# Kernel optimization log

Measured on AMD Instinct MI355X. Metric: run time of the kernel, lower is better.

The kernel has to match this reference:

```python
import jax, jax.numpy as jnp
import numpy as np
from jax import lax

HEADS, DIM_HEAD, LANDMARKS, PINV_ITERS = 8, 64, 256, 6
D = 512


def layernorm(x, w, b, eps=1e-5):
    mu = x.mean(-1, keepdims=True)
    var = ((x - mu) ** 2).mean(-1, keepdims=True)
    return (x - mu) * lax.rsqrt(var + eps) * w + b


def pinv_iter(x, iters=PINV_ITERS):
    # Moore-Penrose pseudo-inverse via Newton-Schulz (lucidrains nystrom-attention)
    abs_x = jnp.abs(x)
    z = jnp.swapaxes(x, -1, -2) / (jnp.max(abs_x.sum(-1)) * jnp.max(abs_x.sum(-2)))
    I = jnp.eye(x.shape[-1], dtype=x.dtype)
    for _ in range(iters):
        xz = x @ z
        z = 0.25 * z @ (13 * I - xz @ (15 * I - xz @ (7 * I - xz)))
    return z


def nystrom_attention(x, qkv_w, out_w, out_b, res_w):
    b, n, _ = x.shape
    m = LANDMARKS
    pad = (m - n % m) % m
    xp = jnp.pad(x, ((0, 0), (pad, 0), (0, 0)))  # left-pad seq to multiple of m
    n_p = n + pad
    q, k, v = jnp.split(xp @ qkv_w, 3, axis=-1)
    split = lambda t: t.reshape(b, n_p, HEADS, DIM_HEAD).transpose(0, 2, 1, 3)
    q, k, v = split(q), split(k), split(v)  # (b, h, n_p, d)
    q = q * DIM_HEAD ** -0.5
    l = n_p // m  # tokens per landmark
    q_l = q.reshape(b, HEADS, m, l, DIM_HEAD).mean(3)  # (b, h, m, d)
    k_l = k.reshape(b, HEADS, m, l, DIM_HEAD).mean(3)
    a1 = jax.nn.softmax(jnp.einsum('bhnd,bhmd->bhnm', q, k_l), -1)  # (b,h,n_p,m)
    a2 = jax.nn.softmax(jnp.einsum('bhmd,bhld->bhml', q_l, k_l), -1)  # (b,h,m,m)
    a3 = jax.nn.softmax(jnp.einsum('bhmd,bhnd->bhmn', q_l, k), -1)  # (b,h,m,n_p)
    out = (a1 @ pinv_iter(a2)) @ (a3 @ v)  # (b,h,n_p,d)
    # depthwise residual conv over the seq dim, kernel (33,1), one per head
    res = lax.conv_general_dilated(v, res_w, (1, 1), [(16, 16), (0, 0)],
                                   dimension_numbers=('NCHW', 'OIHW', 'NCHW'),
                                   feature_group_count=HEADS)
    out = out + res
    out = out.transpose(0, 2, 1, 3).reshape(b, n_p, HEADS * DIM_HEAD)
    return (out @ out_w + out_b)[:, -n:]


def ppeg(x, Hh, Ww, w7, b7, w5, b5, w3, b3):
    B, _, C = x.shape
    cls_tok, feat = x[:, :1], x[:, 1:]
    f = feat.transpose(0, 2, 1).reshape(B, C, Hh, Ww)
    def dwconv(w, bb, p):
        return lax.conv_general_dilated(f, w, (1, 1), [(p, p), (p, p)],
                                        dimension_numbers=('NCHW', 'OIHW', 'NCHW'),
                                        feature_group_count=C) + bb[None, :, None, None]
    y = f + dwconv(w7, b7, 3) + dwconv(w5, b5, 2) + dwconv(w3, b3, 1)
    y = y.reshape(B, C, Hh * Ww).transpose(0, 2, 1)
    return jnp.concatenate([cls_tok, y], axis=1)


def setup_inputs() -> dict:
    key = jax.random.key(0)
    ks = jax.random.split(key, 16)
    E, NC, H = 1024, 4, HEADS
    f32 = jnp.float32
    rn = lambda k, shp, s=0.02: (jax.random.normal(k, shp, f32) * s)
    return {
        'x': jax.random.normal(ks[0], (1, 40960, E), f32),
        'fc1_w': rn(ks[1], (E, D)), 'fc1_b': jnp.zeros((D,), f32),
        'cls_token': jax.random.normal(ks[2], (1, 1, D), f32),
        'l1_norm_w': jnp.ones((D,), f32), 'l1_norm_b': jnp.zeros((D,), f32),
        'l1_qkv_w': rn(ks[3], (D, 3 * D)),
        'l1_out_w': rn(ks[4], (D, D)), 'l1_out_b': jnp.zeros((D,), f32),
        'l1_res_w': rn(ks[5], (H, 1, 33, 1), 0.1),
        'ppeg_w7': rn(ks[6], (D, 1, 7, 7), 0.1), 'ppeg_b7': jnp.zeros((D,), f32),
        'ppeg_w5': rn(ks[7], (D, 1, 5, 5), 0.1), 'ppeg_b5': jnp.zeros((D,), f32),
        'ppeg_w3': rn(ks[8], (D, 1, 3, 3), 0.1), 'ppeg_b3': jnp.zeros((D,), f32),
        'l2_norm_w': jnp.ones((D,), f32), 'l2_norm_b': jnp.zeros((D,), f32),
        'l2_qkv_w': rn(ks[9], (D, 3 * D)),
        'l2_out_w': rn(ks[10], (D, D)), 'l2_out_b': jnp.zeros((D,), f32),
        'l2_res_w': rn(ks[11], (H, 1, 33, 1), 0.1),
        'norm_w': jnp.ones((D,), f32), 'norm_b': jnp.zeros((D,), f32),
        'fc3_w': rn(ks[12], (D, NC)), 'fc3_b': jnp.zeros((NC,), f32),
    }


def reference(x, fc1_w, fc1_b, cls_token, l1_norm_w, l1_norm_b, l1_qkv_w, l1_out_w, l1_out_b, l1_res_w, ppeg_w7, ppeg_b7, ppeg_w5, ppeg_b5, ppeg_w3, ppeg_b3, l2_norm_w, l2_norm_b, l2_qkv_w, l2_out_w, l2_out_b, l2_res_w, norm_w, norm_b, fc3_w, fc3_b):
    B, N, E = x.shape  # (1, 40960, 1024)
    POOL_OUT = 20480
    # AdaptiveMaxPool2d((20480, E)) on a (1, N, E) tensor: max-pool seq dim N -> 20480
    ft = x.reshape(B, POOL_OUT, N // POOL_OUT, E).max(axis=2)
    ft = jax.nn.relu(ft @ fc1_w + fc1_b)  # (1, 20480, 512)
    Hn = ft.shape[1]
    _H = int(np.ceil(np.sqrt(Hn)))  # 144
    add = _H * _H - Hn  # 256
    ft = jnp.concatenate([ft, ft[:, :add]], axis=1)  # (1, 20736, 512)
    h = jnp.concatenate([jnp.broadcast_to(cls_token, (B, 1, D)), ft], axis=1)  # 20737 tokens
    h = h + nystrom_attention(layernorm(h, l1_norm_w, l1_norm_b), l1_qkv_w, l1_out_w, l1_out_b, l1_res_w)
    h = ppeg(h, _H, _H, ppeg_w7, ppeg_b7, ppeg_w5, ppeg_b5, ppeg_w3, ppeg_b3)
    h = h + nystrom_attention(layernorm(h, l2_norm_w, l2_norm_b), l2_qkv_w, l2_out_w, l2_out_b, l2_res_w)
    h = layernorm(h, norm_w, norm_b)[:, 0]
    logits = h @ fc3_w + fc3_b
    return logits, jax.nn.softmax(logits, -1), jnp.argmax(logits, -1)
```

## Files before the change

kernel.cpp:

```cpp
#include <hip/hip_runtime.h>


constexpr int D_    = 512;
constexpr int E_    = 1024;
constexpr int NTOK  = 20737;
constexpr int NP_   = 20992;
constexpr int NH_   = 8;
constexpr int HD_   = 64;
constexpr int MLM   = 256;
constexpr int LCH   = 82;
constexpr int HHW   = 144;
constexpr int NFEAT = 20736;
constexpr int PADR  = 255;
constexpr int NCH   = 41;
constexpr int CHTOK = 512;

typedef __attribute__((ext_vector_type(8))) short bf16x8;
typedef __attribute__((ext_vector_type(4))) float f32x4;

__device__ __forceinline__ unsigned short f2bf(float f){
  unsigned int u = __float_as_uint(f);
  unsigned int r = u + 0x7fffu + ((u >> 16) & 1u);
  return (unsigned short)(r >> 16);
}
__device__ __forceinline__ float bfu(unsigned short u){
  return __uint_as_float((unsigned int)u << 16);
}

__device__ __forceinline__ float waveMaxF(float v){
#pragma unroll
  for (int o = 32; o > 0; o >>= 1) v = fmaxf(v, __shfl_xor(v, o));
  return v;
}
__device__ __forceinline__ float waveSumF(float v){
#pragma unroll
  for (int o = 32; o > 0; o >>= 1) v += __shfl_xor(v, o);
  return v;
}
__device__ __forceinline__ float blockMax256(float v, float* sbuf){
  v = waveMaxF(v);
  if ((threadIdx.x & 63) == 0) sbuf[threadIdx.x >> 6] = v;
  __syncthreads();
  float r = fmaxf(fmaxf(sbuf[0], sbuf[1]), fmaxf(sbuf[2], sbuf[3]));
  __syncthreads();
  return r;
}
__device__ __forceinline__ float blockSum256(float v, float* sbuf){
  v = waveSumF(v);
  if ((threadIdx.x & 63) == 0) sbuf[threadIdx.x >> 6] = v;
  __syncthreads();
  float r = sbuf[0] + sbuf[1] + sbuf[2] + sbuf[3];
  __syncthreads();
  return r;
}

__global__ __launch_bounds__(256) void wtrans_kernel(
    const float* __restrict__ W, unsigned short* __restrict__ Wt, int K, int N){
  __shared__ float tile[32][33];
  const int kb = blockIdx.x * 32, nb = blockIdx.y * 32;
  const int tx = threadIdx.x, ty = threadIdx.y;
  for (int i = ty; i < 32; i += 8) tile[i][tx] = W[(size_t)(kb + i) * N + nb + tx];
  __syncthreads();
  for (int i = ty; i < 32; i += 8)
    Wt[(size_t)(nb + i) * K + kb + tx] = f2bf(tile[tx][i]);
}

__global__ __launch_bounds__(256) void pool_bf16_kernel(
    const float* __restrict__ x, unsigned short* __restrict__ Ah){
  size_t idx4 = ((size_t)blockIdx.x * 256 + threadIdx.x) * 4;
  size_t m = idx4 >> 10, e = idx4 & 1023;
  float4 a = *(const float4*)(x + (m * 2) * E_ + e);
  float4 b = *(const float4*)(x + (m * 2 + 1) * E_ + e);
  unsigned long long pk =
      (unsigned long long)f2bf(fmaxf(a.x, b.x))
    | ((unsigned long long)f2bf(fmaxf(a.y, b.y)) << 16)
    | ((unsigned long long)f2bf(fmaxf(a.z, b.z)) << 32)
    | ((unsigned long long)f2bf(fmaxf(a.w, b.w)) << 48);
  *(unsigned long long*)(Ah + idx4) = pk;
}

__device__ __forceinline__ void mfma_tile64(
    const unsigned short* __restrict__ A, int arows, int bm,
    const unsigned short* __restrict__ Bt, int bn, int K,
    f32x4 acc[2][2], unsigned short* As, unsigned short* Bs){
  const int t = threadIdx.x;
  const int lane = t & 63, wave = t >> 6;
  const int wr = wave >> 1, wc = wave & 1;
  const int m16 = lane & 15, quad = lane >> 4;
  const int srow = t >> 2, scol = (t & 3) * 8;
  for (int kc = 0; kc < K; kc += 32){
    {
      int ga = bm + srow;
      ulonglong2 av = {0ull, 0ull};
      if (ga < arows) av = *(const ulonglong2*)(A + (size_t)ga * K + kc + scol);
      *(ulonglong2*)(As + srow * 40 + scol) = av;
      ulonglong2 bv = *(const ulonglong2*)(Bt + (size_t)(bn + srow) * K + kc + scol);
      *(ulonglong2*)(Bs + srow * 40 + scol) = bv;
    }
    __syncthreads();
    bf16x8 a0 = *(const bf16x8*)(As + (wr * 32 + m16) * 40 + quad * 8);
    bf16x8 a1 = *(const bf16x8*)(As + (wr * 32 + 16 + m16) * 40 + quad * 8);
    bf16x8 b0 = *(const bf16x8*)(Bs + (wc * 32 + m16) * 40 + quad * 8);
    bf16x8 b1 = *(const bf16x8*)(Bs + (wc * 32 + 16 + m16) * 40 + quad * 8);
    acc[0][0] = __builtin_amdgcn_mfma_f32_16x16x32_bf16(a0, b0, acc[0][0], 0, 0, 0);
    acc[0][1] = __builtin_amdgcn_mfma_f32_16x16x32_bf16(a0, b1, acc[0][1], 0, 0, 0);
    acc[1][0] = __builtin_amdgcn_mfma_f32_16x16x32_bf16(a1, b0, acc[1][0], 0, 0, 0);
    acc[1][1] = __builtin_amdgcn_mfma_f32_16x16x32_bf16(a1, b1, acc[1][1], 0, 0, 0);
    __syncthreads();
  }
}

__global__ __launch_bounds__(256) void fc1_mfma_kernel(
    const unsigned short* __restrict__ Ah, const unsigned short* __restrict__ Bt,
    const float* __restrict__ bias, float* __restrict__ h){
  __shared__ unsigned short As[64 * 40], Bs[64 * 40];
  f32x4 z4 = {0.f, 0.f, 0.f, 0.f};
  f32x4 acc[2][2] = {{z4, z4}, {z4, z4}};
  const int bm = blockIdx.x * 64, bn = blockIdx.y * 64;
  mfma_tile64(Ah, 20480, bm, Bt, bn, E_, acc, As, Bs);
  const int lane = threadIdx.x & 63, wave = threadIdx.x >> 6;
  const int wr = wave >> 1, wc = wave & 1;
  const int m16 = lane & 15, quad = lane >> 4;
#pragma unroll
  for (int mi = 0; mi < 2; mi++)
#pragma unroll
    for (int ni = 0; ni < 2; ni++){
      int col = bn + wc * 32 + ni * 16 + m16;
      float bv = bias[col];
#pragma unroll
      for (int r = 0; r < 4; r++){
        int row = bm + wr * 32 + mi * 16 + quad * 4 + r;
        float vv = fmaxf(acc[mi][ni][r] + bv, 0.f);
        h[(size_t)(1 + row) * D_ + col] = vv;
        if (row < 256) h[(size_t)(20481 + row) * D_ + col] = vv;
      }
    }
}

__global__ void cls_kernel(const float* __restrict__ cls, float* __restrict__ h){
  int c = blockIdx.x * 256 + threadIdx.x;
  if (c < D_) h[c] = cls[c];
}

__global__ __launch_bounds__(256) void ln_pad_kernel(
    const float* __restrict__ h, const float* __restrict__ w,
    const float* __restrict__ b, unsigned short* __restrict__ xph){
  const int r = blockIdx.x;
  const int t = threadIdx.x;
  if (r < PADR){
    xph[(size_t)r * D_ + t] = 0;
    xph[(size_t)r * D_ + 256 + t] = 0;
    return;
  }
  __shared__ float s4[4];
  const float* x = h + (size_t)(r - PADR) * D_;
  float a0 = x[t], a1 = x[t + 256];
  float mu = blockSum256(a0 + a1, s4) * (1.f / 512.f);
  float d0 = a0 - mu, d1 = a1 - mu;
  float var = blockSum256(d0 * d0 + d1 * d1, s4) * (1.f / 512.f);
  float rs = rsqrtf(var + 1e-5f);
  xph[(size_t)r * D_ + t]       = f2bf(d0 * rs * w[t] + b[t]);
  xph[(size_t)r * D_ + 256 + t] = f2bf(d1 * rs * w[t + 256] + b[t + 256]);
}

__global__ __launch_bounds__(256) void qkv_mfma_kernel(
    const unsigned short* __restrict__ A, const unsigned short* __restrict__ Bt,
    unsigned short* __restrict__ q16, unsigned short* __restrict__ k16,
    unsigned short* __restrict__ v16){
  __shared__ unsigned short As[64 * 40], Bs[64 * 40];
  f32x4 z4 = {0.f, 0.f, 0.f, 0.f};
  f32x4 acc[2][2] = {{z4, z4}, {z4, z4}};
  const int bm = blockIdx.x * 64, bn = blockIdx.y * 64;
  mfma_tile64(A, NP_, bm, Bt, bn, D_, acc, As, Bs);
  const int lane = threadIdx.x & 63, wave = threadIdx.x >> 6;
  const int wr = wave >> 1, wc = wave & 1;
  const int m16 = lane & 15, quad = lane >> 4;
#pragma unroll
  for (int mi = 0; mi < 2; mi++)
#pragma unroll
    for (int ni = 0; ni < 2; ni++){
      int col = bn + wc * 32 + ni * 16 + m16;
      int which = col >> 9, hh = (col >> 6) & 7, d = col & 63;
      size_t cbase = (size_t)hh * NP_ * HD_ + d;
      unsigned short* dst;
      float sc = 1.f;
      if (which == 0){ dst = q16; sc = 0.125f; }
      else if (which == 1) dst = k16;
      else dst = v16;
#pragma unroll
      for (int r = 0; r < 4; r++){
        int row = bm + wr * 32 + mi * 16 + quad * 4 + r;
        dst[cbase + (size_t)row * HD_] = f2bf(acc[mi][ni][r] * sc);
      }
    }
}

__global__ __launch_bounds__(64) void landmark_kernel(
    const unsigned short* __restrict__ q16, const unsigned short* __restrict__ k16,
    float* __restrict__ ql, float* __restrict__ kl,
    unsigned short* __restrict__ qlh, unsigned short* __restrict__ klh){
  const int im = blockIdx.x, h = blockIdx.y, d = threadIdx.x;
  size_t base = ((size_t)h * NP_ + (size_t)im * LCH) * HD_ + d;
  float sq = 0.f, sk = 0.f;
  for (int r = 0; r < LCH; r++){
    sq += bfu(q16[base + (size_t)r * HD_]);
    sk += bfu(k16[base + (size_t)r * HD_]);
  }
  float qm = sq * (1.f / 82.f), km = sk * (1.f / 82.f);
  size_t oidx = ((size_t)h * MLM + im) * HD_ + d;
  ql[oidx] = qm;  qlh[oidx] = f2bf(qm);
  kl[oidx] = km;  klh[oidx] = f2bf(km);
}

__global__ __launch_bounds__(256) void a2_kernel(
    const float* __restrict__ ql, const float* __restrict__ kl,
    float* __restrict__ a2){
  const int im = blockIdx.x, h = blockIdx.y, t = threadIdx.x;
  __shared__ __align__(16) float qs[64];
  __shared__ float s4[4];
  if (t < 64) qs[t] = ql[((size_t)h * MLM + im) * HD_ + t];
  __syncthreads();
  const float4* kr4 = (const float4*)(kl + ((size_t)h * MLM + t) * HD_);
  const float4* qs4 = (const float4*)qs;
  float s = 0.f;
#pragma unroll
  for (int d4 = 0; d4 < 16; d4++){
    float4 kv = kr4[d4], qv = qs4[d4];
    s += qv.x*kv.x + qv.y*kv.y + qv.z*kv.z + qv.w*kv.w;
  }
  float mx = blockMax256(s, s4);
  float e = __expf(s - mx);
  float S = blockSum256(e, s4);
  a2[((size_t)h * MLM + im) * MLM + t] = e / S;
}

__global__ void zero2_kernel(unsigned int* p){ if (threadIdx.x < 2) p[threadIdx.x] = 0u; }

__global__ __launch_bounds__(256) void pinv_scale_kernel(
    const float* __restrict__ a2, unsigned int* __restrict__ scal){
  const int h = blockIdx.x, j = threadIdx.x;
  const float* A = a2 + (size_t)h * MLM * MLM;
  float rs = 0.f, cs = 0.f;
  for (int t = 0; t < MLM; t++){
    rs += fabsf(A[(size_t)j * MLM + t]);
    cs += fabsf(A[(size_t)t * MLM + j]);
  }
  __shared__ float s4[4];
  float rmax = blockMax256(rs, s4);
  float cmax = blockMax256(cs, s4);
  if (j == 0){
    atomicMax(&scal[0], __float_as_uint(rmax));
    atomicMax(&scal[1], __float_as_uint(cmax));
  }
}

__global__ __launch_bounds__(256) void pinv_init_kernel(
    const float* __restrict__ a2, const unsigned int* __restrict__ scal,
    float* __restrict__ z){
  const int i = blockIdx.x, h = blockIdx.y, j = threadIdx.x;
  float inv = 1.f / (__uint_as_float(scal[0]) * __uint_as_float(scal[1]));
  z[((size_t)h * MLM + i) * MLM + j] = a2[((size_t)h * MLM + j) * MLM + i] * inv;
}

__global__ __launch_bounds__(256) void bmm256_mfma_kernel(
    const float* __restrict__ Ab, const float* __restrict__ Bb,
    float* __restrict__ Cb, float c0, float sgn, float c1){
  __shared__ unsigned short Ash[64 * 40], Asl[64 * 40];
  __shared__ unsigned short Bsh[64 * 40], Bsl[64 * 40];
  const int h = blockIdx.z;
  const float* A = Ab + (size_t)h * 65536;
  const float* B = Bb + (size_t)h * 65536;
  float* C = Cb + (size_t)h * 65536;
  const int bm = blockIdx.x * 64, bn = blockIdx.y * 64;
  const int t = threadIdx.x, lane = t & 63, w = t >> 6;
  const int wr = w >> 1, wc = w & 1, m16 = lane & 15, quad = lane >> 4;
  f32x4 z4 = {0.f, 0.f, 0.f, 0.f};
  f32x4 acc[2][2] = {{z4, z4}, {z4, z4}};
  for (int kc = 0; kc < 256; kc += 32){
    {
      int row = t >> 2, c8 = (t & 3) * 8;
      const float* src = A + (size_t)(bm + row) * 256 + kc + c8;
      float xs[8];
      *(float4*)(xs)     = *(const float4*)src;
      *(float4*)(xs + 4) = *(const float4*)(src + 4);
#pragma unroll
      for (int j = 0; j < 8; j++){
        unsigned short hi = f2bf(xs[j]);
        Ash[row * 40 + c8 + j] = hi;
        Asl[row * 40 + c8 + j] = f2bf(xs[j] - bfu(hi));
      }
      int k = t >> 3, n8 = (t & 7) * 8;
      const float* bsrc = B + (size_t)(kc + k) * 256 + bn + n8;
      float ys[8];
      *(float4*)(ys)     = *(const float4*)bsrc;
      *(float4*)(ys + 4) = *(const float4*)(bsrc + 4);
#pragma unroll
      for (int j = 0; j < 8; j++){
        float xv = sgn * ys[j];
        if (kc + k == bn + n8 + j) xv += c0;
        unsigned short hi = f2bf(xv);
        Bsh[(n8 + j) * 40 + k] = hi;
        Bsl[(n8 + j) * 40 + k] = f2bf(xv - bfu(hi));
      }
    }
    __syncthreads();
    bf16x8 ah[2], al[2], bh[2], bl[2];
#pragma unroll
    for (int mi = 0; mi < 2; mi++){
      ah[mi] = *(const bf16x8*)(Ash + (wr * 32 + mi * 16 + m16) * 40 + quad * 8);
      al[mi] = *(const bf16x8*)(Asl + (wr * 32 + mi * 16 + m16) * 40 + quad * 8);
      bh[mi] = *(const bf16x8*)(Bsh + (wc * 32 + mi * 16 + m16) * 40 + quad * 8);
      bl[mi] = *(const bf16x8*)(Bsl + (wc * 32 + mi * 16 + m16) * 40 + quad * 8);
    }
#pragma unroll
    for (int mi = 0; mi < 2; mi++)
#pragma unroll
      for (int ni = 0; ni < 2; ni++){
        acc[mi][ni] = __builtin_amdgcn_mfma_f32_16x16x32_bf16(ah[mi], bh[ni], acc[mi][ni], 0, 0, 0);
        acc[mi][ni] = __builtin_amdgcn_mfma_f32_16x16x32_bf16(ah[mi], bl[ni], acc[mi][ni], 0, 0, 0);
        acc[mi][ni] = __builtin_amdgcn_mfma_f32_16x16x32_bf16(al[mi], bh[ni], acc[mi][ni], 0, 0, 0);
      }
    __syncthreads();
  }
#pragma unroll
  for (int mi = 0; mi < 2; mi++)
#pragma unroll
    for (int ni = 0; ni < 2; ni++)
#pragma unroll
      for (int r = 0; r < 4; r++){
        int row = bm + wr * 32 + mi * 16 + quad * 4 + r;
        int col = bn + wc * 32 + ni * 16 + m16;
        C[(size_t)row * 256 + col] = c1 * acc[mi][ni][r];
      }
}

__global__ __launch_bounds__(256) void a3v_part_kernel(
    const unsigned short* __restrict__ qlh, const unsigned short* __restrict__ k16,
    const unsigned short* __restrict__ v16, float* __restrict__ pacc,
    float* __restrict__ pml){
  __shared__ __align__(16) unsigned short qs16[64 * 72];
  __shared__ __align__(16) unsigned short kb16[64 * 72];
  __shared__ __align__(16) unsigned short vt16[64 * 72];
  const int lt = blockIdx.x, h = blockIdx.y, ch = blockIdx.z;
  const int t = threadIdx.x;
  const int lane = t & 63, w = t >> 6;
  const int m16 = lane & 15, quad = lane >> 4;

  const unsigned short* qg = qlh + ((size_t)h * MLM + lt * 64) * HD_;
  for (int idx = t; idx < 512; idx += 256){
    int row = idx >> 3, off = (idx & 7) * 8;
    *(uint4*)(qs16 + row * 72 + off) = *(const uint4*)(qg + (size_t)row * HD_ + off);
  }
  f32x4 z4 = {0.f, 0.f, 0.f, 0.f};
  f32x4 acc_o[4] = {z4, z4, z4, z4};
  float mreg[4], lreg[4];
#pragma unroll
  for (int r = 0; r < 4; r++){ mreg[r] = -3.0e38f; lreg[r] = 0.f; }
  const unsigned short* kg = k16 + ((size_t)h * NP_ + ch * CHTOK) * HD_;
  const unsigned short* vg = v16 + ((size_t)h * NP_ + ch * CHTOK) * HD_;

  for (int sc = 0; sc < 8; sc++){
    __syncthreads();
    for (int idx = t; idx < 512; idx += 256){
      int row = idx >> 3, off = (idx & 7) * 8;
      *(uint4*)(kb16 + row * 72 + off) =
          *(const uint4*)(kg + (size_t)(sc * 64 + row) * HD_ + off);
      uint4 pv = *(const uint4*)(vg + (size_t)(sc * 64 + row) * HD_ + off);
      unsigned int uu[4] = {pv.x, pv.y, pv.z, pv.w};
#pragma unroll
      for (int j = 0; j < 4; j++){
        vt16[(off + 2 * j)     * 72 + row] = (unsigned short)(uu[j] & 0xffffu);
        vt16[(off + 2 * j + 1) * 72 + row] = (unsigned short)(uu[j] >> 16);
      }
    }
    __syncthreads();
    f32x4 acc_s[4] = {z4, z4, z4, z4};
#pragma unroll
    for (int kc = 0; kc < 64; kc += 32){
      bf16x8 a = *(const bf16x8*)(qs16 + (w * 16 + m16) * 72 + kc + quad * 8);
#pragma unroll
      for (int ni = 0; ni < 4; ni++){
        bf16x8 b = *(const bf16x8*)(kb16 + (ni * 16 + m16) * 72 + kc + quad * 8);
        acc_s[ni] = __builtin_amdgcn_mfma_f32_16x16x32_bf16(a, b, acc_s[ni], 0, 0, 0);
      }
    }
    __syncthreads();
#pragma unroll
    for (int r = 0; r < 4; r++){
      float cm = fmaxf(fmaxf(acc_s[0][r], acc_s[1][r]), fmaxf(acc_s[2][r], acc_s[3][r]));
#pragma unroll
      for (int o = 1; o < 16; o <<= 1) cm = fmaxf(cm, __shfl_xor(cm, o));
      float mn = fmaxf(mreg[r], cm);
      float scl = __expf(mreg[r] - mn);
      float p0 = __expf(acc_s[0][r] - mn), p1 = __expf(acc_s[1][r] - mn);
      float p2 = __expf(acc_s[2][r] - mn), p3 = __expf(acc_s[3][r] - mn);
      float ls = (p0 + p1) + (p2 + p3);
#pragma unroll
      for (int o = 1; o < 16; o <<= 1) ls += __shfl_xor(ls, o);
      lreg[r] = lreg[r] * scl + ls;
      mreg[r] = mn;
      acc_o[0][r] *= scl; acc_o[1][r] *= scl;
      acc_o[2][r] *= scl; acc_o[3][r] *= scl;
      int prow = (w * 16 + quad * 4 + r) * 72 + m16;
      kb16[prow + 0]  = f2bf(p0);
      kb16[prow + 16] = f2bf(p1);
      kb16[prow + 32] = f2bf(p2);
      kb16[prow + 48] = f2bf(p3);
    }
    __syncthreads();
#pragma unroll
    for (int kc = 0; kc < 64; kc += 32){
      bf16x8 a = *(const bf16x8*)(kb16 + (w * 16 + m16) * 72 + kc + quad * 8);
#pragma unroll
      for (int ni = 0; ni < 4; ni++){
        bf16x8 b = *(const bf16x8*)(vt16 + (ni * 16 + m16) * 72 + kc + quad * 8);
        acc_o[ni] = __builtin_amdgcn_mfma_f32_16x16x32_bf16(a, b, acc_o[ni], 0, 0, 0);
      }
    }
  }
#pragma unroll
  for (int r = 0; r < 4; r++){
    int im = lt * 64 + w * 16 + quad * 4 + r;
    size_t base = ((size_t)h * NCH + ch) * MLM + im;
#pragma unroll
    for (int ni = 0; ni < 4; ni++)
      pacc[base * HD_ + ni * 16 + m16] = acc_o[ni][r];
    if (m16 == 0){
      pml[base * 2]     = mreg[r];
      pml[base * 2 + 1] = lreg[r];
    }
  }
}

__global__ __launch_bounds__(64) void a3v_combine_kernel(
    const float* __restrict__ pacc, const float* __restrict__ pml,
    float* __restrict__ t1){
  const int im = blockIdx.x, h = blockIdx.y, lane = threadIdx.x;
  float M = -3.0e38f;
  for (int c = 0; c < NCH; c++)
    M = fmaxf(M, pml[(((size_t)h * NCH + c) * MLM + im) * 2]);
  float accv = 0.f, L = 0.f;
  for (int c = 0; c < NCH; c++){
    size_t base = ((size_t)h * NCH + c) * MLM + im;
    float mc = pml[base * 2], lc = pml[base * 2 + 1];
    float w = __expf(mc - M);
    accv += w * pacc[base * HD_ + lane];
    L += w * lc;
  }
  t1[((size_t)h * MLM + im) * HD_ + lane] = accv / L;
}

__global__ __launch_bounds__(256) void zt1_kernel(
    const float* __restrict__ z, const float* __restrict__ t1,
    unsigned short* __restrict__ t2t){
  const int h = blockIdx.y;
  const int t = threadIdx.x;
  const int d = t & 63, ri = t >> 6;
  const int im = blockIdx.x * 4 + ri;
  const float* zr = z + ((size_t)h * MLM + im) * MLM;
  const float* t1h = t1 + (size_t)h * MLM * HD_;
  float acc = 0.f;
#pragma unroll 8
  for (int kk = 0; kk < MLM; kk++) acc += zr[kk] * t1h[(size_t)kk * HD_ + d];
  t2t[((size_t)h * HD_ + d) * MLM + im] = f2bf(acc);
}

__global__ __launch_bounds__(256) void out_tile_kernel(
    const unsigned short* __restrict__ q16, const unsigned short* __restrict__ klh,
    const unsigned short* __restrict__ t2t, const unsigned short* __restrict__ v16,
    const float* __restrict__ resw, unsigned short* __restrict__ outh){
  __shared__ __align__(16) unsigned short smem[64 * 72 * 2 + 64 * 264];
  unsigned short* qs16 = smem;
  unsigned short* kb16 = smem + 64 * 72;
  unsigned short* Ps   = smem + 64 * 72 * 2;
  const int tile = blockIdx.x, h = blockIdx.y;
  const int n0 = PADR + tile * 64;
  const int t = threadIdx.x;
  const int lane = t & 63, w = t >> 6;
  const int m16 = lane & 15, quad = lane >> 4;

  {
    const unsigned short* qh = q16 + (size_t)h * NP_ * HD_;
    for (int idx = t; idx < 512; idx += 256){
      int row = idx >> 3, off = (idx & 7) * 8;
      int n = n0 + row;
      uint4 val = {0u, 0u, 0u, 0u};
      if (n < NP_) val = *(const uint4*)(qh + (size_t)n * HD_ + off);
      *(uint4*)(qs16 + row * 72 + off) = val;
    }
  }
  f32x4 z4 = {0.f, 0.f, 0.f, 0.f};
  f32x4 acc_s[16];
#pragma unroll
  for (int i = 0; i < 16; i++) acc_s[i] = z4;
  const unsigned short* klg = klh + (size_t)h * MLM * HD_;
  for (int m = 0; m < 4; m++){
    __syncthreads();
    for (int idx = t; idx < 512; idx += 256){
      int row = idx >> 3, off = (idx & 7) * 8;
      *(uint4*)(kb16 + row * 72 + off) =
          *(const uint4*)(klg + (size_t)(m * 64 + row) * HD_ + off);
    }
    __syncthreads();
#pragma unroll
    for (int kc = 0; kc < 64; kc += 32){
      bf16x8 a = *(const bf16x8*)(qs16 + (w * 16 + m16) * 72 + kc + quad * 8);
#pragma unroll
      for (int ni = 0; ni < 4; ni++){
        bf16x8 b = *(const bf16x8*)(kb16 + (ni * 16 + m16) * 72 + kc + quad * 8);
        acc_s[m * 4 + ni] = __builtin_amdgcn_mfma_f32_16x16x32_bf16(a, b, acc_s[m * 4 + ni], 0, 0, 0);
      }
    }
  }
  __syncthreads();
#pragma unroll
  for (int r = 0; r < 4; r++){
    float mx = acc_s[0][r];
#pragma unroll
    for (int mc = 1; mc < 16; mc++) mx = fmaxf(mx, acc_s[mc][r]);
#pragma unroll
    for (int o = 1; o < 16; o <<= 1) mx = fmaxf(mx, __shfl_xor(mx, o));
    float p[16]; float sum = 0.f;
#pragma unroll
    for (int mc = 0; mc < 16; mc++){ p[mc] = __expf(acc_s[mc][r] - mx); sum += p[mc]; }
#pragma unroll
    for (int o = 1; o < 16; o <<= 1) sum += __shfl_xor(sum, o);
    float inv = 1.f / sum;
    int prow = (w * 16 + quad * 4 + r) * 264;
#pragma unroll
    for (int mc = 0; mc < 16; mc++)
      Ps[prow + (mc >> 2) * 64 + (mc & 3) * 16 + m16] = f2bf(p[mc] * inv);
  }
  f32x4 acc_o[4] = {z4, z4, z4, z4};
  const unsigned short* t2g = t2t + (size_t)h * HD_ * MLM;
  for (int ch = 0; ch < 4; ch++){
    __syncthreads();
    {
      int row = t >> 2, c8 = (t & 3) * 16;
      const unsigned short* src = t2g + (size_t)row * MLM + ch * 64 + c8;
      *(uint4*)(kb16 + row * 72 + c8)     = *(const uint4*)src;
      *(uint4*)(kb16 + row * 72 + c8 + 8) = *(const uint4*)(src + 8);
    }
    __syncthreads();
#pragma unroll
    for (int kc = 0; kc < 64; kc += 32){
      bf16x8 a = *(const bf16x8*)(Ps + (w * 16 + m16) * 264 + ch * 64 + kc + quad * 8);
#pragma unroll
      for (int ni = 0; ni < 4; ni++){
        bf16x8 b = *(const bf16x8*)(kb16 + (ni * 16 + m16) * 72 + kc + quad * 8);
        acc_o[ni] = __builtin_amdgcn_mfma_f32_16x16x32_bf16(a, b, acc_o[ni], 0, 0, 0);
      }
    }
  }
  __syncthreads();
  float* Obuf = (float*)Ps;
  unsigned short* vtile = (unsigned short*)(Obuf + 64 * 66);
#pragma unroll
  for (int r = 0; r < 4; r++){
    int row = w * 16 + quad * 4 + r;
#pragma unroll
    for (int ni = 0; ni < 4; ni++)
      Obuf[row * 66 + ni * 16 + m16] = acc_o[ni][r];
  }
  {
    const unsigned short* vh = v16 + (size_t)h * NP_ * HD_;
    for (int idx = t; idx < 768; idx += 256){
      int row = idx >> 3, off = (idx & 7) * 8;
      int nn = n0 - 16 + row;
      uint4 val = {0u, 0u, 0u, 0u};
      if (nn < NP_) val = *(const uint4*)(vh + (size_t)nn * HD_ + off);
      *(uint4*)(vtile + row * 72 + off) = val;
    }
  }
  __syncthreads();
  float wreg[33];
  {
    const float* wr = resw + h * 33;
#pragma unroll
    for (int kk = 0; kk < 33; kk++) wreg[kk] = wr[kk];
  }
  const int ty = t >> 4, tx = t & 15;
#pragma unroll
  for (int i = 0; i < 4; i++){
    int lrow = ty * 4 + i;
    float c0v = 0.f, c1v = 0.f, c2v = 0.f, c3v = 0.f;
    for (int kk = 0; kk < 33; kk++){
      uint2 uv = *(const uint2*)(vtile + (lrow + kk) * 72 + tx * 4);
      float wv = wreg[kk];
      c0v += __uint_as_float(uv.x << 16) * wv;
      c1v += __uint_as_float(uv.x & 0xffff0000u) * wv;
      c2v += __uint_as_float(uv.y << 16) * wv;
      c3v += __uint_as_float(uv.y & 0xffff0000u) * wv;
    }
    int trow = tile * 64 + lrow;
    if (trow < NTOK){
      const float* orow = Obuf + lrow * 66 + tx * 4;
      unsigned long long pk =
          (unsigned long long)f2bf(orow[0] + c0v)
        | ((unsigned long long)f2bf(orow[1] + c1v) << 16)
        | ((unsigned long long)f2bf(orow[2] + c2v) << 32)
        | ((unsigned long long)f2bf(orow[3] + c3v) << 48);
      *(unsigned long long*)(outh + (size_t)trow * D_ + h * HD_ + tx * 4) = pk;
    }
  }
}

__global__ __launch_bounds__(256) void proj_mfma_kernel(
    const unsigned short* __restrict__ A, const unsigned short* __restrict__ Bt,
    const float* __restrict__ bias, float* __restrict__ h){
  __shared__ unsigned short As[64 * 40], Bs[64 * 40];
  f32x4 z4 = {0.f, 0.f, 0.f, 0.f};
  f32x4 acc[2][2] = {{z4, z4}, {z4, z4}};
  const int bm = blockIdx.x * 64, bn = blockIdx.y * 64;
  mfma_tile64(A, NTOK, bm, Bt, bn, D_, acc, As, Bs);
  const int lane = threadIdx.x & 63, wave = threadIdx.x >> 6;
  const int wr = wave >> 1, wc = wave & 1;
  const int m16 = lane & 15, quad = lane >> 4;
#pragma unroll
  for (int mi = 0; mi < 2; mi++)
#pragma unroll
    for (int ni = 0; ni < 2; ni++){
      int col = bn + wc * 32 + ni * 16 + m16;
      float bv = bias[col];
#pragma unroll
      for (int r = 0; r < 4; r++){
        int row = bm + wr * 32 + mi * 16 + quad * 4 + r;
        if (row < NTOK) h[(size_t)row * D_ + col] += acc[mi][ni][r] + bv;
      }
    }
}

__global__ __launch_bounds__(512) void ppeg_combine_kernel(
    const float* __restrict__ w7, const float* __restrict__ b7,
    const float* __restrict__ w5, const float* __restrict__ b5,
    const float* __restrict__ w3, const float* __restrict__ b3,
    float* __restrict__ wcomb, float* __restrict__ bcomb){
  const int c = threadIdx.x;
#pragma unroll
  for (int i = 0; i < 7; i++){
#pragma unroll
    for (int j = 0; j < 7; j++){
      int di = i - 3, dj = j - 3;
      float wv = w7[(size_t)c * 49 + i * 7 + j];
      if (di >= -2 && di <= 2 && dj >= -2 && dj <= 2)
        wv += w5[(size_t)c * 25 + (di + 2) * 5 + (dj + 2)];
      if (di >= -1 && di <= 1 && dj >= -1 && dj <= 1)
        wv += w3[(size_t)c * 9 + (di + 1) * 3 + (dj + 1)];
      if (di == 0 && dj == 0) wv += 1.f;
      wcomb[(size_t)(i * 7 + j) * 512 + c] = wv;
    }
  }
  bcomb[c] = b7[c] + b5[c] + b3[c];
}

__global__ __launch_bounds__(512) void ppeg_conv_kernel(
    const float* __restrict__ h, const float* __restrict__ wcomb,
    const float* __restrict__ bcomb, float* __restrict__ tmp){
  const int c = threadIdx.x;
  const int y = blockIdx.y;
  const int x0 = blockIdx.x * 8;
  float wc[49];
#pragma unroll
  for (int kk = 0; kk < 49; kk++) wc[kk] = wcomb[(size_t)kk * 512 + c];
  float acc[8];
  const float bv = bcomb[c];
#pragma unroll
  for (int p = 0; p < 8; p++) acc[p] = bv;
#pragma unroll
  for (int i = 0; i < 7; i++){
    const int yy = y + i - 3;
    if (yy < 0 || yy >= HHW) continue;
    const float* hrow = h + (size_t)(1 + yy * HHW) * D_ + c;
    float line[14];
#pragma unroll
    for (int j = 0; j < 14; j++){
      const int xx = x0 + j - 3;
      line[j] = (xx >= 0 && xx < HHW) ? hrow[(size_t)xx * D_] : 0.f;
    }
#pragma unroll
    for (int p = 0; p < 8; p++)
#pragma unroll
      for (int j = 0; j < 7; j++)
        acc[p] += line[p + j] * wc[i * 7 + j];
  }
#pragma unroll
  for (int p = 0; p < 8; p++)
    tmp[(size_t)(y * HHW + x0 + p) * D_ + c] = acc[p];
}

__global__ void ppeg_copy_kernel(const float* __restrict__ tmp, float* __restrict__ h){
  size_t idx = (size_t)blockIdx.x * 256 + threadIdx.x;
  if (idx < (size_t)NFEAT * D_) h[idx + D_] = tmp[idx];
}

__global__ __launch_bounds__(512) void final_kernel(
    const float* __restrict__ h, const float* __restrict__ w,
    const float* __restrict__ b, const float* __restrict__ fc3w,
    const float* __restrict__ fc3b, float* __restrict__ out){
  __shared__ float vec[512];
  __shared__ float s8[8];
  __shared__ float lg[4];
  const int t = threadIdx.x;
  float x = h[t];
  float v = waveSumF(x);
  if ((t & 63) == 0) s8[t >> 6] = v;
  __syncthreads();
  float sum = 0.f;
#pragma unroll
  for (int i = 0; i < 8; i++) sum += s8[i];
  float mu = sum * (1.f / 512.f);
  __syncthreads();
  float d = x - mu;
  v = waveSumF(d * d);
  if ((t & 63) == 0) s8[t >> 6] = v;
  __syncthreads();
  float var = 0.f;
#pragma unroll
  for (int i = 0; i < 8; i++) var += s8[i];
  var *= (1.f / 512.f);
  float rs = rsqrtf(var + 1e-5f);
  vec[t] = d * rs * w[t] + b[t];
  __syncthreads();
  if (t < 4){
    float acc = fc3b[t];
    for (int kk = 0; kk < 512; kk++) acc += vec[kk] * fc3w[kk * 4 + t];
    lg[t] = acc;
  }
  __syncthreads();
  if (t == 0){
    float m = fmaxf(fmaxf(lg[0], lg[1]), fmaxf(lg[2], lg[3]));
    float e[4], se = 0.f;
#pragma unroll
    for (int i = 0; i < 4; i++){ e[i] = __expf(lg[i] - m); se += e[i]; }
    int am = 0; float bm = lg[0];
#pragma unroll
    for (int i = 1; i < 4; i++) if (lg[i] > bm){ bm = lg[i]; am = i; }
#pragma unroll
    for (int i = 0; i < 4; i++){ out[i] = lg[i]; out[4 + i] = e[i] / se; }
    out[8] = (float)am;
  }
}

extern "C" void kernel_launch(void* const* d_in, const int* in_sizes, int n_in,
                              void* d_out, int out_size, void* d_ws, size_t ws_size,
                              hipStream_t stream) {
  const float* x       = (const float*)d_in[0];
  const float* fc1_w   = (const float*)d_in[1];
  const float* fc1_b   = (const float*)d_in[2];
  const float* cls_tok = (const float*)d_in[3];
  const float* l1_nw   = (const float*)d_in[4];
  const float* l1_nb   = (const float*)d_in[5];
  const float* l1_qkvw = (const float*)d_in[6];
  const float* l1_outw = (const float*)d_in[7];
  const float* l1_outb = (const float*)d_in[8];
  const float* l1_resw = (const float*)d_in[9];
  const float* ppeg_w7 = (const float*)d_in[10];
  const float* ppeg_b7 = (const float*)d_in[11];
  const float* ppeg_w5 = (const float*)d_in[12];
  const float* ppeg_b5 = (const float*)d_in[13];
  const float* ppeg_w3 = (const float*)d_in[14];
  const float* ppeg_b3 = (const float*)d_in[15];
  const float* l2_nw   = (const float*)d_in[16];
  const float* l2_nb   = (const float*)d_in[17];
  const float* l2_qkvw = (const float*)d_in[18];
  const float* l2_outw = (const float*)d_in[19];
  const float* l2_outb = (const float*)d_in[20];
  const float* l2_resw = (const float*)d_in[21];
  const float* norm_w  = (const float*)d_in[22];
  const float* norm_b  = (const float*)d_in[23];
  const float* fc3_w   = (const float*)d_in[24];
  const float* fc3_b   = (const float*)d_in[25];

  float* W = (float*)d_ws;
  size_t o = 0;
  float* hbuf = W + o; o += (size_t)NTOK * D_;
  float* xp   = W + o; o += (size_t)NP_ * D_;
  float* qb   = W + o; o += (size_t)NH_ * NP_ * HD_;
  float* kb   = W + o; o += (size_t)NH_ * NP_ * HD_;
  float* vb   = W + o; o += (size_t)NH_ * NP_ * HD_;
  float* qlb  = W + o; o += (size_t)NH_ * MLM * HD_;
  float* klb  = W + o; o += (size_t)NH_ * MLM * HD_;
  float* a2b  = W + o; o += (size_t)NH_ * MLM * MLM;
  float* z0   = W + o; o += (size_t)NH_ * MLM * MLM;
  float* z1   = W + o; o += (size_t)NH_ * MLM * MLM;
  float* ta   = W + o; o += (size_t)NH_ * MLM * MLM;
  float* tb   = W + o; o += (size_t)NH_ * MLM * MLM;
  float* tc   = W + o; o += (size_t)NH_ * MLM * MLM;
  float* t1b  = W + o; o += (size_t)NH_ * MLM * HD_;
  float* t2r  = W + o; o += (size_t)NH_ * MLM * HD_;
  unsigned int* scal = (unsigned int*)(W + o); o += 16;
  float* wcomb = W + o; o += 49 * 512;
  float* bcomb = W + o; o += 512;
  unsigned short* fc1_wt  = (unsigned short*)(W + o); o += (size_t)D_ * E_ / 2;
  unsigned short* qkv_wt1 = (unsigned short*)(W + o); o += (size_t)1536 * D_ / 2;
  unsigned short* qkv_wt2 = (unsigned short*)(W + o); o += (size_t)1536 * D_ / 2;
  unsigned short* out_wt1 = (unsigned short*)(W + o); o += (size_t)D_ * D_ / 2;
  unsigned short* out_wt2 = (unsigned short*)(W + o); o += (size_t)D_ * D_ / 2;
  unsigned short* qlh = (unsigned short*)(W + o); o += (size_t)NH_ * MLM * HD_ / 2;
  unsigned short* klh = (unsigned short*)(W + o); o += (size_t)NH_ * MLM * HD_ / 2;

  unsigned short* xph = (unsigned short*)xp;
  float* pacc = xp;
  float* pml  = xp + (size_t)NH_ * NCH * MLM * HD_;
  unsigned short* outh = (unsigned short*)xp;
  unsigned short* Ah  = (unsigned short*)qb;
  unsigned short* q16 = (unsigned short*)qb;
  unsigned short* k16 = (unsigned short*)kb;
  unsigned short* v16 = (unsigned short*)vb;
  unsigned short* t2t = (unsigned short*)t2r;

  wtrans_kernel<<<dim3(E_ / 32, D_ / 32), dim3(32, 8), 0, stream>>>(fc1_w, fc1_wt, E_, D_);
  wtrans_kernel<<<dim3(D_ / 32, 1536 / 32), dim3(32, 8), 0, stream>>>(l1_qkvw, qkv_wt1, D_, 1536);
  wtrans_kernel<<<dim3(D_ / 32, 1536 / 32), dim3(32, 8), 0, stream>>>(l2_qkvw, qkv_wt2, D_, 1536);
  wtrans_kernel<<<dim3(D_ / 32, D_ / 32), dim3(32, 8), 0, stream>>>(l1_outw, out_wt1, D_, D_);
  wtrans_kernel<<<dim3(D_ / 32, D_ / 32), dim3(32, 8), 0, stream>>>(l2_outw, out_wt2, D_, D_);
  ppeg_combine_kernel<<<1, 512, 0, stream>>>(ppeg_w7, ppeg_b7, ppeg_w5, ppeg_b5,
                                             ppeg_w3, ppeg_b3, wcomb, bcomb);

  pool_bf16_kernel<<<20480, 256, 0, stream>>>(x, Ah);
  fc1_mfma_kernel<<<dim3(320, 8), 256, 0, stream>>>(Ah, fc1_wt, fc1_b, hbuf);
  cls_kernel<<<2, 256, 0, stream>>>(cls_tok, hbuf);

  auto run_layer = [&](const float* nw, const float* nb,
                       const unsigned short* qkvwt, const unsigned short* outwt,
                       const float* outb, const float* resw){
    ln_pad_kernel<<<NP_, 256, 0, stream>>>(hbuf, nw, nb, xph);
    qkv_mfma_kernel<<<dim3(328, 24), 256, 0, stream>>>(xph, qkvwt, q16, k16, v16);
    landmark_kernel<<<dim3(256, 8), 64, 0, stream>>>(q16, k16, qlb, klb, qlh, klh);
    a2_kernel<<<dim3(256, 8), 256, 0, stream>>>(qlb, klb, a2b);
    zero2_kernel<<<1, 64, 0, stream>>>(scal);
    pinv_scale_kernel<<<8, 256, 0, stream>>>(a2b, scal);
    pinv_init_kernel<<<dim3(256, 8), 256, 0, stream>>>(a2b, scal, z0);
    float* zc = z0; float* za = z1;
    for (int it = 0; it < 6; it++){
      bmm256_mfma_kernel<<<dim3(4, 4, 8), 256, 0, stream>>>(a2b, zc, ta, 0.f, 1.f, 1.f);
      bmm256_mfma_kernel<<<dim3(4, 4, 8), 256, 0, stream>>>(ta, ta, tb, 7.f, -1.f, 1.f);
      bmm256_mfma_kernel<<<dim3(4, 4, 8), 256, 0, stream>>>(ta, tb, tc, 15.f, -1.f, 1.f);
      bmm256_mfma_kernel<<<dim3(4, 4, 8), 256, 0, stream>>>(zc, tc, za, 13.f, -1.f, 0.25f);
      float* tswap = zc; zc = za; za = tswap;
    }
    a3v_part_kernel<<<dim3(4, 8, NCH), 256, 0, stream>>>(qlh, k16, v16, pacc, pml);
    a3v_combine_kernel<<<dim3(256, 8), 64, 0, stream>>>(pacc, pml, t1b);
    zt1_kernel<<<dim3(64, 8), 256, 0, stream>>>(zc, t1b, t2t);
    out_tile_kernel<<<dim3(325, 8), 256, 0, stream>>>(q16, klh, t2t, v16, resw, outh);
    proj_mfma_kernel<<<dim3(325, 8), 256, 0, stream>>>(outh, outwt, outb, hbuf);
  };

  run_layer(l1_nw, l1_nb, qkv_wt1, out_wt1, l1_outb, l1_resw);
  ppeg_conv_kernel<<<dim3(HHW / 8, HHW), 512, 0, stream>>>(hbuf, wcomb, bcomb, xp);
  ppeg_copy_kernel<<<(NFEAT * D_ + 255) / 256, 256, 0, stream>>>(xp, hbuf);
  run_layer(l2_nw, l2_nb, qkv_wt2, out_wt2, l2_outb, l2_resw);
  final_kernel<<<1, 512, 0, stream>>>(hbuf, norm_w, norm_b, fc3_w, fc3_b, (float*)d_out);
}
```

Before: 1.735 ms.

## Fuse pinv iterations into one cooperative kernel and widen GEMM K-step

Replaces the 27 separate launches for the Newton-Schulz pseudo-inverse (zeroing, scale, init, 24 bmm launches) with a single cooperative kernel of 128 blocks that uses grid.sync between stages, removing launch gaps and the atomic scale reduction. Separately, the shared bf16 MFMA tile routine now stages a K-chunk of 64 instead of 32, which halves the number of barriers per tile at the cost of more LDS per block. After an even number of iterations the result ends in z0, so zt1 reads z0 directly. Grid-wide syncs across a small grid add their own latency.

```diff
diff --git a/kernel.cpp b/kernel.cpp
--- a/kernel.cpp
+++ b/kernel.cpp
@@ -1,5 +1,8 @@
 #include <hip/hip_runtime.h>
-
+#include <hip/hip_cooperative_groups.h>
+
+
+namespace cg = cooperative_groups;
 
 constexpr int D_    = 512;
 constexpr int E_    = 1024;
@@ -87,25 +90,28 @@
   const int lane = t & 63, wave = t >> 6;
   const int wr = wave >> 1, wc = wave & 1;
   const int m16 = lane & 15, quad = lane >> 4;
-  const int srow = t >> 2, scol = (t & 3) * 8;
-  for (int kc = 0; kc < K; kc += 32){
-    {
-      int ga = bm + srow;
+  for (int kc = 0; kc < K; kc += 64){
+    for (int idx = t; idx < 512; idx += 256){
+      int row = idx >> 3, off = (idx & 7) * 8;
+      int ga = bm + row;
       ulonglong2 av = {0ull, 0ull};
-      if (ga < arows) av = *(const ulonglong2*)(A + (size_t)ga * K + kc + scol);
-      *(ulonglong2*)(As + srow * 40 + scol) = av;
-      ulonglong2 bv = *(const ulonglong2*)(Bt + (size_t)(bn + srow) * K + kc + scol);
-      *(ulonglong2*)(Bs + srow * 40 + scol) = bv;
-    }
-    __syncthreads();
-    bf16x8 a0 = *(const bf16x8*)(As + (wr * 32 + m16) * 40 + quad * 8);
-    bf16x8 a1 = *(const bf16x8*)(As + (wr * 32 + 16 + m16) * 40 + quad * 8);
-    bf16x8 b0 = *(const bf16x8*)(Bs + (wc * 32 + m16) * 40 + quad * 8);
-    bf16x8 b1 = *(const bf16x8*)(Bs + (wc * 32 + 16 + m16) * 40 + quad * 8);
-    acc[0][0] = __builtin_amdgcn_mfma_f32_16x16x32_bf16(a0, b0, acc[0][0], 0, 0, 0);
-    acc[0][1] = __builtin_amdgcn_mfma_f32_16x16x32_bf16(a0, b1, acc[0][1], 0, 0, 0);
-    acc[1][0] = __builtin_amdgcn_mfma_f32_16x16x32_bf16(a1, b0, acc[1][0], 0, 0, 0);
-    acc[1][1] = __builtin_amdgcn_mfma_f32_16x16x32_bf16(a1, b1, acc[1][1], 0, 0, 0);
+      if (ga < arows) av = *(const ulonglong2*)(A + (size_t)ga * K + kc + off);
+      *(ulonglong2*)(As + row * 72 + off) = av;
+      ulonglong2 bv = *(const ulonglong2*)(Bt + (size_t)(bn + row) * K + kc + off);
+      *(ulonglong2*)(Bs + row * 72 + off) = bv;
+    }
+    __syncthreads();
+#pragma unroll
+    for (int k2 = 0; k2 < 64; k2 += 32){
+      bf16x8 a0 = *(const bf16x8*)(As + (wr * 32 + m16) * 72 + k2 + quad * 8);
+      bf16x8 a1 = *(const bf16x8*)(As + (wr * 32 + 16 + m16) * 72 + k2 + quad * 8);
+      bf16x8 b0 = *(const bf16x8*)(Bs + (wc * 32 + m16) * 72 + k2 + quad * 8);
+      bf16x8 b1 = *(const bf16x8*)(Bs + (wc * 32 + 16 + m16) * 72 + k2 + quad * 8);
+      acc[0][0] = __builtin_amdgcn_mfma_f32_16x16x32_bf16(a0, b0, acc[0][0], 0, 0, 0);
+      acc[0][1] = __builtin_amdgcn_mfma_f32_16x16x32_bf16(a0, b1, acc[0][1], 0, 0, 0);
+      acc[1][0] = __builtin_amdgcn_mfma_f32_16x16x32_bf16(a1, b0, acc[1][0], 0, 0, 0);
+      acc[1][1] = __builtin_amdgcn_mfma_f32_16x16x32_bf16(a1, b1, acc[1][1], 0, 0, 0);
+    }
     __syncthreads();
   }
 }
@@ -113,7 +119,7 @@
 __global__ __launch_bounds__(256) void fc1_mfma_kernel(
     const unsigned short* __restrict__ Ah, const unsigned short* __restrict__ Bt,
     const float* __restrict__ bias, float* __restrict__ h){
-  __shared__ unsigned short As[64 * 40], Bs[64 * 40];
+  __shared__ unsigned short As[64 * 72], Bs[64 * 72];
   f32x4 z4 = {0.f, 0.f, 0.f, 0.f};
   f32x4 acc[2][2] = {{z4, z4}, {z4, z4}};
   const int bm = blockIdx.x * 64, bn = blockIdx.y * 64;
@@ -167,7 +173,7 @@
     const unsigned short* __restrict__ A, const unsigned short* __restrict__ Bt,
     unsigned short* __restrict__ q16, unsigned short* __restrict__ k16,
     unsigned short* __restrict__ v16){
-  __shared__ unsigned short As[64 * 40], Bs[64 * 40];
+  __shared__ unsigned short As[64 * 72], Bs[64 * 72];
   f32x4 z4 = {0.f, 0.f, 0.f, 0.f};
   f32x4 acc[2][2] = {{z4, z4}, {z4, z4}};
   const int bm = blockIdx.x * 64, bn = blockIdx.y * 64;
@@ -234,44 +240,17 @@
   a2[((size_t)h * MLM + im) * MLM + t] = e / S;
 }
 
-__global__ void zero2_kernel(unsigned int* p){ if (threadIdx.x < 2) p[threadIdx.x] = 0u; }
-
-__global__ __launch_bounds__(256) void pinv_scale_kernel(
-    const float* __restrict__ a2, unsigned int* __restrict__ scal){
-  const int h = blockIdx.x, j = threadIdx.x;
-  const float* A = a2 + (size_t)h * MLM * MLM;
-  float rs = 0.f, cs = 0.f;
-  for (int t = 0; t < MLM; t++){
-    rs += fabsf(A[(size_t)j * MLM + t]);
-    cs += fabsf(A[(size_t)t * MLM + j]);
-  }
-  __shared__ float s4[4];
-  float rmax = blockMax256(rs, s4);
-  float cmax = blockMax256(cs, s4);
-  if (j == 0){
-    atomicMax(&scal[0], __float_as_uint(rmax));
-    atomicMax(&scal[1], __float_as_uint(cmax));
-  }
-}
-
-__global__ __launch_bounds__(256) void pinv_init_kernel(
-    const float* __restrict__ a2, const unsigned int* __restrict__ scal,
-    float* __restrict__ z){
-  const int i = blockIdx.x, h = blockIdx.y, j = threadIdx.x;
-  float inv = 1.f / (__uint_as_float(scal[0]) * __uint_as_float(scal[1]));
-  z[((size_t)h * MLM + i) * MLM + j] = a2[((size_t)h * MLM + j) * MLM + i] * inv;
-}
-
-__global__ __launch_bounds__(256) void bmm256_mfma_kernel(
+__device__ __forceinline__ void bmm_stage(
     const float* __restrict__ Ab, const float* __restrict__ Bb,
-    float* __restrict__ Cb, float c0, float sgn, float c1){
-  __shared__ unsigned short Ash[64 * 40], Asl[64 * 40];
-  __shared__ unsigned short Bsh[64 * 40], Bsl[64 * 40];
-  const int h = blockIdx.z;
+    float* __restrict__ Cb, float c0, float sgn, float c1,
+    unsigned short* Ash, unsigned short* Asl,
+    unsigned short* Bsh, unsigned short* Bsl){
+  const int blk = blockIdx.x;
+  const int h = blk >> 4, tile = blk & 15;
+  const int bm = (tile >> 2) * 64, bn = (tile & 3) * 64;
   const float* A = Ab + (size_t)h * 65536;
   const float* B = Bb + (size_t)h * 65536;
   float* C = Cb + (size_t)h * 65536;
-  const int bm = blockIdx.x * 64, bn = blockIdx.y * 64;
   const int t = threadIdx.x, lane = t & 63, w = t >> 6;
   const int wr = w >> 1, wc = w & 1, m16 = lane & 15, quad = lane >> 4;
   f32x4 z4 = {0.f, 0.f, 0.f, 0.f};
@@ -332,6 +311,57 @@
         int col = bn + wc * 32 + ni * 16 + m16;
         C[(size_t)row * 256 + col] = c1 * acc[mi][ni][r];
       }
+}
+
+__global__ __launch_bounds__(256) void pinv_coop_kernel(
+    const float* __restrict__ a2, float* __restrict__ z0, float* __restrict__ z1,
+    float* __restrict__ ta, float* __restrict__ tb, float* __restrict__ tc,
+    float* __restrict__ scal){
+  __shared__ __align__(16) unsigned short Ash[64 * 40], Asl[64 * 40];
+  __shared__ __align__(16) unsigned short Bsh[64 * 40], Bsl[64 * 40];
+  cg::grid_group grid = cg::this_grid();
+  const int blk = blockIdx.x, t = threadIdx.x;
+
+  if (blk < 8){
+    const float* A = a2 + (size_t)blk * 65536;
+    float rs = 0.f, cs = 0.f;
+    for (int k = 0; k < 256; k++){
+      rs += fabsf(A[(size_t)t * 256 + k]);
+      cs += fabsf(A[(size_t)k * 256 + t]);
+    }
+    float* sb = (float*)Ash;
+    float rmax = blockMax256(rs, sb);
+    float cmax = blockMax256(cs, sb);
+    if (t == 0){ scal[blk * 2] = rmax; scal[blk * 2 + 1] = cmax; }
+  }
+  grid.sync();
+  {
+    float rmax = scal[0], cmax = scal[1];
+#pragma unroll
+    for (int h = 1; h < 8; h++){
+      rmax = fmaxf(rmax, scal[h * 2]);
+      cmax = fmaxf(cmax, scal[h * 2 + 1]);
+    }
+    float inv = 1.f / (rmax * cmax);
+    int h = blk >> 4, t16 = blk & 15;
+    const float* A = a2 + (size_t)h * 65536;
+    float* Z = z0 + (size_t)h * 65536;
+    for (int idx = t; idx < 4096; idx += 256){
+      int i = t16 * 16 + (idx >> 8);
+      int j = idx & 255;
+      Z[(size_t)i * 256 + j] = A[(size_t)j * 256 + i] * inv;
+    }
+  }
+  grid.sync();
+  float* zc = z0; float* za = z1;
+  for (int it = 0; it < 6; it++){
+    bmm_stage(a2, zc, ta, 0.f, 1.f, 1.f, Ash, Asl, Bsh, Bsl);   grid.sync();
+    bmm_stage(ta, ta, tb, 7.f, -1.f, 1.f, Ash, Asl, Bsh, Bsl);  grid.sync();
+    bmm_stage(ta, tb, tc, 15.f, -1.f, 1.f, Ash, Asl, Bsh, Bsl); grid.sync();
+    bmm_stage(zc, tc, za, 13.f, -1.f, 0.25f, Ash, Asl, Bsh, Bsl);
+    float* tmp = zc; zc = za; za = tmp;
+    if (it < 5) grid.sync();
+  }
 }
 
 __global__ __launch_bounds__(256) void a3v_part_kernel(
@@ -608,7 +638,7 @@
 __global__ __launch_bounds__(256) void proj_mfma_kernel(
     const unsigned short* __restrict__ A, const unsigned short* __restrict__ Bt,
     const float* __restrict__ bias, float* __restrict__ h){
-  __shared__ unsigned short As[64 * 40], Bs[64 * 40];
+  __shared__ unsigned short As[64 * 72], Bs[64 * 72];
   f32x4 z4 = {0.f, 0.f, 0.f, 0.f};
   f32x4 acc[2][2] = {{z4, z4}, {z4, z4}};
   const int bm = blockIdx.x * 64, bn = blockIdx.y * 64;
@@ -788,7 +818,7 @@
   float* tc   = W + o; o += (size_t)NH_ * MLM * MLM;
   float* t1b  = W + o; o += (size_t)NH_ * MLM * HD_;
   float* t2r  = W + o; o += (size_t)NH_ * MLM * HD_;
-  unsigned int* scal = (unsigned int*)(W + o); o += 16;
+  float* scalf = W + o; o += 16;
   float* wcomb = W + o; o += 49 * 512;
   float* bcomb = W + o; o += 512;
   unsigned short* fc1_wt  = (unsigned short*)(W + o); o += (size_t)D_ * E_ / 2;
@@ -828,20 +858,15 @@
     qkv_mfma_kernel<<<dim3(328, 24), 256, 0, stream>>>(xph, qkvwt, q16, k16, v16);
     landmark_kernel<<<dim3(256, 8), 64, 0, stream>>>(q16, k16, qlb, klb, qlh, klh);
     a2_kernel<<<dim3(256, 8), 256, 0, stream>>>(qlb, klb, a2b);
-    zero2_kernel<<<1, 64, 0, stream>>>(scal);
-    pinv_scale_kernel<<<8, 256, 0, stream>>>(a2b, scal);
-    pinv_init_kernel<<<dim3(256, 8), 256, 0, stream>>>(a2b, scal, z0);
-    float* zc = z0; float* za = z1;
-    for (int it = 0; it < 6; it++){
-      bmm256_mfma_kernel<<<dim3(4, 4, 8), 256, 0, stream>>>(a2b, zc, ta, 0.f, 1.f, 1.f);
-      bmm256_mfma_kernel<<<dim3(4, 4, 8), 256, 0, stream>>>(ta, ta, tb, 7.f, -1.f, 1.f);
-      bmm256_mfma_kernel<<<dim3(4, 4, 8), 256, 0, stream>>>(ta, tb, tc, 15.f, -1.f, 1.f);
-      bmm256_mfma_kernel<<<dim3(4, 4, 8), 256, 0, stream>>>(zc, tc, za, 13.f, -1.f, 0.25f);
-      float* tswap = zc; zc = za; za = tswap;
+    {
+      void* args[] = {(void*)&a2b, (void*)&z0, (void*)&z1,
+                      (void*)&ta, (void*)&tb, (void*)&tc, (void*)&scalf};
+      hipLaunchCooperativeKernel((void*)pinv_coop_kernel, dim3(128), dim3(256),
+                                 args, 0, stream);
     }
     a3v_part_kernel<<<dim3(4, 8, NCH), 256, 0, stream>>>(qlh, k16, v16, pacc, pml);
     a3v_combine_kernel<<<dim3(256, 8), 64, 0, stream>>>(pacc, pml, t1b);
-    zt1_kernel<<<dim3(64, 8), 256, 0, stream>>>(zc, t1b, t2t);
+    zt1_kernel<<<dim3(64, 8), 256, 0, stream>>>(z0, t1b, t2t);
     out_tile_kernel<<<dim3(325, 8), 256, 0, stream>>>(q16, klh, t2t, v16, resw, outh);
     proj_mfma_kernel<<<dim3(325, 8), 256, 0, stream>>>(outh, outwt, outb, hbuf);
   };
```

New measurement: 2.500 ms. 1.44x slower.
